# Performance work log

Measured on AMD Instinct MI355X. Metric: run time of the kernel, lower is better.

## Reference

```python
import jax, jax.numpy as jnp
import numpy as np

H = 128  # lstm_hidden_dim


def setup_inputs() -> dict:
    key = jax.random.key(0)
    ks = jax.random.split(key, 7)
    T, B, D = 512, 1024, 128
    s = 1.0 / np.sqrt(H)  # pytorch default LSTM init scale
    return {
        "inp": jax.random.normal(ks[0], (T, B, D), dtype=jnp.float32),
        "W_ih": jax.random.uniform(ks[1], (4 * H, D), jnp.float32, -s, s),
        "W_hh": jax.random.uniform(ks[2], (4 * H, H), jnp.float32, -s, s),
        "b_ih": jax.random.uniform(ks[3], (4 * H,), jnp.float32, -s, s),
        "b_hh": jax.random.uniform(ks[4], (4 * H,), jnp.float32, -s, s),
        "W_lin": jax.random.uniform(ks[5], (H, H), jnp.float32, -s, s),
        "b_lin": jax.random.uniform(ks[6], (H,), jnp.float32, -s, s),
        "future": 128,
    }


def _lstm_cell(x, h, c, W_ih, W_hh, b_ih, b_hh):
    # gates: [B, 4H], PyTorch gate order i, f, g, o
    gates = x @ W_ih.T + b_ih + h @ W_hh.T + b_hh
    i, f, g, o = jnp.split(gates, 4, axis=-1)
    i, f, o = jax.nn.sigmoid(i), jax.nn.sigmoid(f), jax.nn.sigmoid(o)
    g = jnp.tanh(g)
    c_new = f * c + i * g
    h_new = o * jnp.tanh(c_new)
    return h_new, c_new


def reference(inp, W_ih, W_hh, b_ih, b_hh, W_lin, b_lin, future):
    B = inp.shape[1]
    h0 = jnp.zeros((B, H), inp.dtype)
    c0 = jnp.zeros((B, H), inp.dtype)

    def scan_step(carry, x):
        h, c = carry
        h, c = _lstm_cell(x, h, c, W_ih, W_hh, b_ih, b_hh)
        return (h, c), None

    (h, c), _ = jax.lax.scan(scan_step, (h0, c0), inp)
    out = h @ W_lin.T + b_lin  # [B, H]

    def fut_step(carry, _):
        o, h, c = carry
        h, c = _lstm_cell(o, h, c, W_ih, W_hh, b_ih, b_hh)
        o = h @ W_lin.T + b_lin
        return (o, h, c), o

    (_, _, _), fut_outs = jax.lax.scan(fut_step, (out, h, c), None, length=future)
    # outputs: [future + 1, B, H]
    return jnp.concatenate([out[None], fut_outs], axis=0)
```

## Files before the change

### kernel.cpp

```cpp
#include <hip/hip_runtime.h>

#define TSTEPS 512
#define BATCH  1024
#define DIM    128
#define HID    128
#define FUT    128
#define BTILE  4
#define NBLOCKS (BATCH / BTILE)
#define NTHREADS 512
#define LSTR   136

typedef __bf16 bf16x8 __attribute__((ext_vector_type(8)));
typedef float  f32x4  __attribute__((ext_vector_type(4)));
typedef unsigned int uint32x2 __attribute__((ext_vector_type(2)));

#define LOG2E 1.4426950408889634f

#if defined(__has_builtin)
#if __has_builtin(__builtin_amdgcn_permlane16_swap) && __has_builtin(__builtin_amdgcn_permlane32_swap)
#define HAVE_PERMSWAP 1
#endif
#endif
#ifndef HAVE_PERMSWAP
#define HAVE_PERMSWAP 0
#endif

__device__ __forceinline__ bf16x8 ldfrag(const float* __restrict__ p) {
    f32x4 a = *(const f32x4*)p;
    f32x4 b = *(const f32x4*)(p + 4);
    bf16x8 r;
    r[0] = (__bf16)a[0]; r[1] = (__bf16)a[1]; r[2] = (__bf16)a[2]; r[3] = (__bf16)a[3];
    r[4] = (__bf16)b[0]; r[5] = (__bf16)b[1]; r[6] = (__bf16)b[2]; r[7] = (__bf16)b[3];
    return r;
}

__device__ __forceinline__ float cell_update(f32x4 gv, float& c) {
    float pi = gv[0], pf = gv[1], pg = gv[2], po = gv[3];
    float ti = __builtin_amdgcn_exp2f(-LOG2E        * __builtin_fabsf(pi));
    float tf = __builtin_amdgcn_exp2f(-LOG2E        * __builtin_fabsf(pf));
    float tg = __builtin_amdgcn_exp2f(-2.0f * LOG2E * __builtin_fabsf(pg));
    float to = __builtin_amdgcn_exp2f(-LOG2E        * __builtin_fabsf(po));
    float di = 1.0f + ti, df = 1.0f + tf, dg = 1.0f + tg, dox = 1.0f + to;
    float p1 = di * df, p2 = dg * dox;
    float invP  = __builtin_amdgcn_rcpf(p1 * p2);
    float inv12 = invP * p2;
    float inv34 = invP * p1;
    float ig = ((pi >= 0.0f) ? 1.0f : ti) * (inv12 * df);
    float fg = ((pf >= 0.0f) ? 1.0f : tf) * (inv12 * di);
    float og = ((po >= 0.0f) ? 1.0f : to) * (inv34 * dg);
    float gg = __builtin_copysignf((1.0f - tg) * (inv34 * dox), pg);
    c = fg * c + ig * gg;
    float tc  = __builtin_amdgcn_exp2f(-2.0f * LOG2E * __builtin_fabsf(c));
    float thc = __builtin_copysignf((1.0f - tc) * __builtin_amdgcn_rcpf(1.0f + tc), c);
    return og * thc;
}

__device__ __forceinline__ float sel4(int q, float b0, float b1, float b2, float b3) {
    float lo = (q & 1) ? b1 : b0;
    float hi = (q & 1) ? b3 : b2;
    return (q & 2) ? hi : lo;
}

#if HAVE_PERMSWAP
__device__ __forceinline__ float gate_gather_perm(f32x4 a, bool r1_16, bool r1_32) {
    uint32x2 s01 = __builtin_amdgcn_permlane16_swap(__float_as_uint(a[0]), __float_as_uint(a[1]), false, false);
    uint32x2 s23 = __builtin_amdgcn_permlane16_swap(__float_as_uint(a[2]), __float_as_uint(a[3]), false, false);
    unsigned lo = r1_16 ? s01[1] : s01[0];
    unsigned hi = r1_16 ? s23[1] : s23[0];
    uint32x2 fin = __builtin_amdgcn_permlane32_swap(lo, hi, false, false);
    return __uint_as_float(r1_32 ? fin[1] : fin[0]);
}
#endif

__global__ __launch_bounds__(NTHREADS, 2)
void lstm_forecast(const float* __restrict__ inp,
                   const float* __restrict__ W_ih, const float* __restrict__ W_hh,
                   const float* __restrict__ b_ih, const float* __restrict__ b_hh,
                   const float* __restrict__ W_lin, const float* __restrict__ b_lin,
                   float* __restrict__ out)
{
    __shared__ __bf16 x_sh[2][16 * LSTR];
    __shared__ __bf16 h_sh[2][16 * LSTR];

    const int tid  = threadIdx.x;
    const int lane = tid & 63;
    const int wave = tid >> 6;
    const int q    = lane >> 4;
    const int m    = lane & 15;
    const int bo   = blockIdx.x * BTILE;

    for (int i = tid; i < 16 * LSTR; i += NTHREADS) {
        x_sh[0][i] = (__bf16)0.0f;
        x_sh[1][i] = (__bf16)0.0f;
        h_sh[0][i] = (__bf16)0.0f;
        h_sh[1][i] = (__bf16)0.0f;
    }

    bool use_perm = false, r1_16 = false, r1_32 = false;
    int  fmap = 0;
#if HAVE_PERMSWAP
    {
        unsigned lid = (unsigned)lane;
        uint32x2 t16 = __builtin_amdgcn_permlane16_swap(lid, lid + 1000u, false, false);
        unsigned v16 = (unsigned)__builtin_amdgcn_readlane((int)t16[0], 0);
        uint32x2 t32 = __builtin_amdgcn_permlane32_swap(lid, lid + 1000u, false, false);
        unsigned v32 = (unsigned)__builtin_amdgcn_readlane((int)t32[0], 0);
        bool ok16 = (v16 == 0u) || (v16 == 16u) || (v16 == 1000u) || (v16 == 1016u);
        bool ok32 = (v32 == 0u) || (v32 == 32u) || (v32 == 1000u) || (v32 == 1032u);
        r1_16 = (v16 == 16u) || (v16 == 1016u);
        r1_32 = (v32 == 32u) || (v32 == 1032u);
        bool fl16 = (v16 >= 1000u);
        bool fl32 = (v32 >= 1000u);
        use_perm = ok16 && ok32;
        fmap = (fl16 ? 1 : 0) | (fl32 ? 2 : 0);
    }
#endif

    bf16x8 wih[4][4], whh[4][4], wlin[4];
    float  bias_g[4];
    #pragma unroll
    for (int g = 0; g < 4; ++g) {
        const int n = g * HID + wave * 16 + m;
        bias_g[g] = b_ih[n] + b_hh[n];
        #pragma unroll
        for (int kt = 0; kt < 4; ++kt) {
            wih[g][kt] = ldfrag(W_ih + (size_t)n * DIM + kt * 32 + q * 8);
            whh[g][kt] = ldfrag(W_hh + (size_t)n * HID + kt * 32 + q * 8);
        }
    }
    const int   nl     = wave * 16 + m;
    const float bias_l = b_lin[nl];
    #pragma unroll
    for (int kt = 0; kt < 4; ++kt)
        wlin[kt] = ldfrag(W_lin + (size_t)nl * HID + kt * 32 + q * 8);

    const int rb = use_perm ? (q ^ fmap) : q;
    const int jj = wave * 16 + m;
    float creg = 0.0f;

    const int lk    = m * LSTR + q * 8;
    const int paddr = (lane & 15) << 2;

    const int cr = tid >> 7, cc = tid & 127;
    const float* xptr = inp + (size_t)(bo + cr) * DIM + cc;
    const size_t XS = (size_t)BATCH * DIM;

    float bank0[8], bank1[8];
    #pragma unroll
    for (int k = 0; k < 8; ++k) {
        bank0[k] = xptr[(size_t)k * XS];
        bank1[k] = xptr[(size_t)(8 + k) * XS];
    }

    __syncthreads();

    for (int tb = 0; tb < TSTEPS; tb += 16) {
        #pragma unroll
        for (int j = 0; j < 16; ++j) {
            const int p = j & 1;
            float xv = (j < 8) ? bank0[j] : bank1[j - 8];
            x_sh[p][cr * LSTR + cc] = (__bf16)xv;
            __syncthreads();

            if (j == 7) {
                if (tb + 16 < TSTEPS) {
                    #pragma unroll
                    for (int k = 0; k < 8; ++k)
                        bank0[k] = xptr[(size_t)(tb + 16 + k) * XS];
                }
            }
            if (j == 15) {
                if (tb + 24 < TSTEPS) {
                    #pragma unroll
                    for (int k = 0; k < 8; ++k)
                        bank1[k] = xptr[(size_t)(tb + 24 + k) * XS];
                }
            }

            f32x4 acc[4];
            #pragma unroll
            for (int g = 0; g < 4; ++g)
                acc[g] = (f32x4){bias_g[g], bias_g[g], bias_g[g], bias_g[g]};
            #pragma unroll
            for (int kt = 0; kt < 4; ++kt) {
                bf16x8 ax = *(const bf16x8*)&x_sh[p][lk + kt * 32];
                bf16x8 ah = *(const bf16x8*)&h_sh[p][lk + kt * 32];
                #pragma unroll
                for (int g = 0; g < 4; ++g) {
                    acc[g] = __builtin_amdgcn_mfma_f32_16x16x32_bf16(ax, wih[g][kt], acc[g], 0, 0, 0);
                    acc[g] = __builtin_amdgcn_mfma_f32_16x16x32_bf16(ah, whh[g][kt], acc[g], 0, 0, 0);
                }
            }

            f32x4 gv;
#if HAVE_PERMSWAP
            if (use_perm) {
                #pragma unroll
                for (int g = 0; g < 4; ++g)
                    gv[g] = gate_gather_perm(acc[g], r1_16, r1_32);
            } else
#endif
            {
                #pragma unroll
                for (int g = 0; g < 4; ++g) {
                    float b0 = __int_as_float(__builtin_amdgcn_ds_bpermute(paddr, __float_as_int(acc[g][0])));
                    float b1 = __int_as_float(__builtin_amdgcn_ds_bpermute(paddr, __float_as_int(acc[g][1])));
                    float b2 = __int_as_float(__builtin_amdgcn_ds_bpermute(paddr, __float_as_int(acc[g][2])));
                    float b3 = __int_as_float(__builtin_amdgcn_ds_bpermute(paddr, __float_as_int(acc[g][3])));
                    gv[g] = sel4(q, b0, b1, b2, b3);
                }
            }

            float h = cell_update(gv, creg);
            h_sh[p ^ 1][rb * LSTR + jj] = (__bf16)h;
        }
    }

    int ph = 0;
    for (int tf = 0; tf <= FUT; ++tf) {
        __syncthreads();
        f32x4 accl = (f32x4){bias_l, bias_l, bias_l, bias_l};
        #pragma unroll
        for (int kt = 0; kt < 4; ++kt) {
            bf16x8 ah = *(const bf16x8*)&h_sh[ph][lk + kt * 32];
            accl = __builtin_amdgcn_mfma_f32_16x16x32_bf16(ah, wlin[kt], accl, 0, 0, 0);
        }
        if (q == 0) {
            #pragma unroll
            for (int r = 0; r < 4; ++r) {
                float o = accl[r];
                out[(size_t)tf * BATCH * HID + (size_t)(bo + r) * HID + nl] = o;
                if (tf < FUT) {
                    __bf16 hi = (__bf16)o;
                    x_sh[0][r * LSTR + nl] = hi;
                    x_sh[1][r * LSTR + nl] = (__bf16)(o - (float)hi);
                }
            }
        }
        if (tf == FUT) break;
        __syncthreads();

        f32x4 acc[4];
        #pragma unroll
        for (int g = 0; g < 4; ++g)
            acc[g] = (f32x4){bias_g[g], bias_g[g], bias_g[g], bias_g[g]};
        #pragma unroll
        for (int kt = 0; kt < 4; ++kt) {
            bf16x8 axh = *(const bf16x8*)&x_sh[0][lk + kt * 32];
            bf16x8 axl = *(const bf16x8*)&x_sh[1][lk + kt * 32];
            bf16x8 ah  = *(const bf16x8*)&h_sh[ph][lk + kt * 32];
            #pragma unroll
            for (int g = 0; g < 4; ++g) {
                acc[g] = __builtin_amdgcn_mfma_f32_16x16x32_bf16(axh, wih[g][kt], acc[g], 0, 0, 0);
                acc[g] = __builtin_amdgcn_mfma_f32_16x16x32_bf16(axl, wih[g][kt], acc[g], 0, 0, 0);
                acc[g] = __builtin_amdgcn_mfma_f32_16x16x32_bf16(ah,  whh[g][kt], acc[g], 0, 0, 0);
            }
        }
        f32x4 gv;
#if HAVE_PERMSWAP
        if (use_perm) {
            #pragma unroll
            for (int g = 0; g < 4; ++g)
                gv[g] = gate_gather_perm(acc[g], r1_16, r1_32);
        } else
#endif
        {
            #pragma unroll
            for (int g = 0; g < 4; ++g) {
                float b0 = __int_as_float(__builtin_amdgcn_ds_bpermute(paddr, __float_as_int(acc[g][0])));
                float b1 = __int_as_float(__builtin_amdgcn_ds_bpermute(paddr, __float_as_int(acc[g][1])));
                float b2 = __int_as_float(__builtin_amdgcn_ds_bpermute(paddr, __float_as_int(acc[g][2])));
                float b3 = __int_as_float(__builtin_amdgcn_ds_bpermute(paddr, __float_as_int(acc[g][3])));
                gv[g] = sel4(q, b0, b1, b2, b3);
            }
        }

        float h = cell_update(gv, creg);
        h_sh[ph ^ 1][rb * LSTR + jj] = (__bf16)h;
        ph ^= 1;
    }
}

extern "C" void kernel_launch(void* const* d_in, const int* in_sizes, int n_in,
                              void* d_out, int out_size, void* d_ws, size_t ws_size,
                              hipStream_t stream) {
    const float* inp   = (const float*)d_in[0];
    const float* W_ih  = (const float*)d_in[1];
    const float* W_hh  = (const float*)d_in[2];
    const float* b_ih  = (const float*)d_in[3];
    const float* b_hh  = (const float*)d_in[4];
    const float* W_lin = (const float*)d_in[5];
    const float* b_lin = (const float*)d_in[6];
    float* out = (float*)d_out;

    hipLaunchKernelGGL(lstm_forecast, dim3(NBLOCKS), dim3(NTHREADS), 0, stream,
                       inp, W_ih, W_hh, b_ih, b_hh, W_lin, b_lin, out);
}
```

Measured before the change: 919.8 us.

## Batch input projection over four timesteps in one MFMA pass

The input-to-hidden projection is no longer computed every step. Every fourth step, four timesteps of x are packed into the 16 M-rows of the MFMA tile, and one set of MFMAs computes x@W_ih for all four steps. Each step then adds its slice of those results after the gate gather, so the serial recurrence only has to do the h@W_hh MFMAs. This halves the MFMA work on the critical path. The cost is extra LDS row mapping through the permutation map, extra registers for the held accumulators, and a zeroing pass on x_sh before the future phase.

Result: faster. 845.3 us (-8.1%).

```diff
diff --git a/kernel.cpp b/kernel.cpp
--- a/kernel.cpp
+++ b/kernel.cpp
@@ -144,6 +144,7 @@
     const int cr = tid >> 7, cc = tid & 127;
     const float* xptr = inp + (size_t)(bo + cr) * DIM + cc;
     const size_t XS = (size_t)BATCH * DIM;
+    const int xrowb = 4 * (use_perm ? (cr ^ fmap) : cr);
 
     float bank0[8], bank1[8];
     #pragma unroll
@@ -154,12 +155,19 @@
 
     __syncthreads();
 
+    f32x4 xacc[4];
+
     for (int tb = 0; tb < TSTEPS; tb += 16) {
         #pragma unroll
         for (int j = 0; j < 16; ++j) {
             const int p = j & 1;
-            float xv = (j < 8) ? bank0[j] : bank1[j - 8];
-            x_sh[p][cr * LSTR + cc] = (__bf16)xv;
+            if ((j & 3) == 0) {
+                #pragma unroll
+                for (int k = 0; k < 4; ++k) {
+                    float xv = ((j + k) < 8) ? bank0[j + k] : bank1[j + k - 8];
+                    x_sh[0][(xrowb + k) * LSTR + cc] = (__bf16)xv;
+                }
+            }
             __syncthreads();
 
             if (j == 7) {
@@ -177,19 +185,29 @@
                 }
             }
 
-            f32x4 acc[4];
+            if ((j & 3) == 0) {
+                #pragma unroll
+                for (int g = 0; g < 4; ++g)
+                    xacc[g] = (f32x4){bias_g[g], bias_g[g], bias_g[g], bias_g[g]};
+                #pragma unroll
+                for (int kt = 0; kt < 4; ++kt) {
+                    bf16x8 ax = *(const bf16x8*)&x_sh[0][lk + kt * 32];
+                    #pragma unroll
+                    for (int g = 0; g < 4; ++g)
+                        xacc[g] = __builtin_amdgcn_mfma_f32_16x16x32_bf16(ax, wih[g][kt], xacc[g], 0, 0, 0);
+                }
+            }
+
+            f32x4 hacc[4];
             #pragma unroll
             for (int g = 0; g < 4; ++g)
-                acc[g] = (f32x4){bias_g[g], bias_g[g], bias_g[g], bias_g[g]};
+                hacc[g] = (f32x4){0.0f, 0.0f, 0.0f, 0.0f};
             #pragma unroll
             for (int kt = 0; kt < 4; ++kt) {
-                bf16x8 ax = *(const bf16x8*)&x_sh[p][lk + kt * 32];
                 bf16x8 ah = *(const bf16x8*)&h_sh[p][lk + kt * 32];
                 #pragma unroll
-                for (int g = 0; g < 4; ++g) {
-                    acc[g] = __builtin_amdgcn_mfma_f32_16x16x32_bf16(ax, wih[g][kt], acc[g], 0, 0, 0);
-                    acc[g] = __builtin_amdgcn_mfma_f32_16x16x32_bf16(ah, whh[g][kt], acc[g], 0, 0, 0);
-                }
+                for (int g = 0; g < 4; ++g)
+                    hacc[g] = __builtin_amdgcn_mfma_f32_16x16x32_bf16(ah, whh[g][kt], hacc[g], 0, 0, 0);
             }
 
             f32x4 gv;
@@ -197,17 +215,17 @@
             if (use_perm) {
                 #pragma unroll
                 for (int g = 0; g < 4; ++g)
-                    gv[g] = gate_gather_perm(acc[g], r1_16, r1_32);
+                    gv[g] = gate_gather_perm(hacc[g], r1_16, r1_32) + xacc[g][j & 3];
             } else
 #endif
             {
                 #pragma unroll
                 for (int g = 0; g < 4; ++g) {
-                    float b0 = __int_as_float(__builtin_amdgcn_ds_bpermute(paddr, __float_as_int(acc[g][0])));
-                    float b1 = __int_as_float(__builtin_amdgcn_ds_bpermute(paddr, __float_as_int(acc[g][1])));
-                    float b2 = __int_as_float(__builtin_amdgcn_ds_bpermute(paddr, __float_as_int(acc[g][2])));
-                    float b3 = __int_as_float(__builtin_amdgcn_ds_bpermute(paddr, __float_as_int(acc[g][3])));
-                    gv[g] = sel4(q, b0, b1, b2, b3);
+                    float b0 = __int_as_float(__builtin_amdgcn_ds_bpermute(paddr, __float_as_int(hacc[g][0])));
+                    float b1 = __int_as_float(__builtin_amdgcn_ds_bpermute(paddr, __float_as_int(hacc[g][1])));
+                    float b2 = __int_as_float(__builtin_amdgcn_ds_bpermute(paddr, __float_as_int(hacc[g][2])));
+                    float b3 = __int_as_float(__builtin_amdgcn_ds_bpermute(paddr, __float_as_int(hacc[g][3])));
+                    gv[g] = sel4(q, b0, b1, b2, b3) + xacc[g][j & 3];
                 }
             }
 
@@ -215,6 +233,9 @@
             h_sh[p ^ 1][rb * LSTR + jj] = (__bf16)h;
         }
     }
+
+    for (int i = tid; i < 16 * LSTR; i += NTHREADS)
+        if (i >= 4 * LSTR) x_sh[0][i] = (__bf16)0.0f;
 
     int ph = 0;
     for (int tf = 0; tf <= FUT; ++tf) {
```
